# Performance work log

Hardware: AMD Instinct MI355X
Metric: run time of the kernel (lower is better)

The kernel has to match this reference:

```python
import jax, jax.numpy as jnp
import numpy as np

DENSE_SHAPE = (256, 3, 3, 256)  # (out_channels, kh, kw, in_channels)
STRIDES = (1, 1)


def _unfold_nchw(x, kh, kw, sh, sw):
    """torch.nn.functional.unfold layout: rows ordered (C, kh, kw)."""
    B, C, H, W = x.shape
    oh = (H - kh) // sh + 1
    ow = (W - kw) // sw + 1
    # [B, C, kh*kw, oh, ow]; small python loop over 3x3 kernel taps only
    patches = jnp.stack(
        [x[:, :, i:i + sh * oh:sh, j:j + sw * ow:sw]
         for i in range(kh) for j in range(kw)], axis=2)
    return patches.reshape(B, C * kh * kw, oh * ow), oh, ow


def setup_inputs() -> dict:
    key = jax.random.key(0)
    k1, k2, k3, k4, k5, k6 = jax.random.split(key, 6)
    O, kh, kw, C = DENSE_SHAPE
    nnz = 2048
    inp = jax.random.normal(k1, (4, 128, 128, C), dtype=jnp.float32)
    # per-column index ranges for COO weight indices [nnz, 4]
    io = jax.random.randint(k2, (nnz, 1), 0, O)
    ih = jax.random.randint(k3, (nnz, 1), 0, kh)
    iw = jax.random.randint(k4, (nnz, 1), 0, kw)
    ic = jax.random.randint(k5, (nnz, 1), 0, C)
    weight_indices = jnp.concatenate([io, ih, iw, ic], axis=1).astype(jnp.int64)
    weight_values = jax.random.normal(k6, (nnz,), dtype=jnp.float32)
    return {"input": inp, "weight_indices": weight_indices,
            "weight_values": weight_values}


def reference(input, weight_indices, weight_values):
    O, kh, kw, C = DENSE_SHAPE
    sh, sw = STRIDES
    B = input.shape[0]
    # densify COO weight (duplicates are summed, matching coalesce)
    W = jnp.zeros(DENSE_SHAPE, dtype=weight_values.dtype).at[
        weight_indices[:, 0], weight_indices[:, 1],
        weight_indices[:, 2], weight_indices[:, 3]].add(weight_values)
    x = jnp.transpose(input, (0, 3, 1, 2))  # NHWC -> NCHW
    U, oh, ow = _unfold_nchw(x, kh, kw, sh, sw)  # [B, C*kh*kw, oh*ow]
    # NOTE: faithful to the original: weight flattened in (kh,kw,C) order
    # while unfold rows are in (C,kh,kw) order -- same raw matmul.
    out = jnp.einsum('ok,bkl->bol', W.reshape(O, -1), U)
    out = out.reshape(B, O, oh, ow)
    return jnp.transpose(out, (0, 2, 3, 1))  # -> NHWC
```

## Files before the change

kernel.cpp:

```cpp
#include <hip/hip_runtime.h>
#include <cstdint>

#define H_IN   128
#define W_IN   128
#define C_IN   256
#define O_OUT  256
#define OH     126
#define OW     126

#define TY     16
#define TX     4
#define IR     (TY + 2)
#define ICOLS  (TX + 2)
#define NPIX   (IR * ICOLS)
#define SHW    258
#define IN_HW  (NPIX * SHW)
#define NWAVES 8
#define OPW    32
#define SST    34
#define STG_W  (64 * SST)
#define LDS_BYTES (NWAVES * STG_W * 4)

__global__ void prep_kernel(const int* __restrict__ wi, const float* __restrict__ wv,
                            int nnz, int* __restrict__ sgS, int* __restrict__ sgBase,
                            int2* __restrict__ tab) {
    __shared__ int cnt[256];
    __shared__ int smax[32];
    __shared__ int sbase[33];
    __shared__ int is32;
    const int tid = threadIdx.x;
    cnt[tid] = 0;
    if (tid == 0) is32 = 0;
    __syncthreads();
    int f = 0;
    for (int idx = tid * 2 + 1; idx < nnz * 4; idx += 512) f |= wi[idx];
    if (f) atomicOr(&is32, 1);
    __syncthreads();
    const int stride = is32 ? 4 : 8;
    const int step   = is32 ? 1 : 2;
    for (int e = tid; e < nnz; e += 256)
        atomicAdd(&cnt[wi[e * stride]], 1);
    __syncthreads();
    if (tid < 32) {
        int m = 0;
        for (int k = 0; k < 8; ++k) m = max(m, cnt[tid * 8 + k]);
        smax[tid] = m;
    }
    __syncthreads();
    if (tid == 0) {
        int s = 0;
        for (int i = 0; i < 32; ++i) { sbase[i] = s; s += 8 * smax[i]; }
        sbase[32] = s;
    }
    __syncthreads();
    const int T = sbase[32];
    for (int i = tid; i < T; i += 256) tab[i] = make_int2(0, 0);
    cnt[tid] = 0;
    __syncthreads();
    for (int e = tid; e < nnz; e += 256) {
        int o  = wi[e * stride];
        int h  = wi[e * stride + 1 * step];
        int w_ = wi[e * stride + 2 * step];
        int c  = wi[e * stride + 3 * step];
        int k   = h * 768 + w_ * 256 + c;
        int cp  = k / 9;
        int rem = k - cp * 9;
        int i_  = rem / 3;
        int j_  = rem - i_ * 3;
        int meta2 = (((i_ * ICOLS + j_) * SHW) + cp) * 2;
        int slot = atomicAdd(&cnt[o], 1);
        tab[sbase[o >> 3] + slot * 8 + (o & 7)] = make_int2(meta2, __float_as_int(wv[e]));
    }
    if (tid < 32) sgS[tid] = smax[tid];
    if (tid < 33) sgBase[tid] = sbase[tid];
}

__device__ inline unsigned short rtne_bf16(float f) {
    unsigned u = __float_as_uint(f);
    u += 0x7FFFu + ((u >> 16) & 1u);
    return (unsigned short)(u >> 16);
}

__device__ __forceinline__ float bfld(const char* b, int off) {
    return __uint_as_float(((unsigned)*(const unsigned short*)(b + off)) << 16);
}

__global__ __launch_bounds__(512, 4)
void conv_kernel(const float* __restrict__ in, float* __restrict__ out,
                 const int* __restrict__ sgS, const int* __restrict__ sgBase,
                 const int2* __restrict__ tab) {
    extern __shared__ char smem[];
    unsigned short* ldsH = (unsigned short*)smem;
    float*          ldsF = (float*)smem;

    const int tid  = threadIdx.x;
    const int w    = tid >> 6;
    const int lane = tid & 63;
    const int tx = blockIdx.x, ty = blockIdx.y, b = blockIdx.z;
    const int iy0 = ty * TY, ix0 = tx * TX;
    const float* inb = in + (size_t)b * (H_IN * W_IN * C_IN);

    for (int p = w; p < NPIX; p += NWAVES) {
        int r = p / ICOLS, c = p - r * ICOLS;
        int gy = iy0 + r, gx = ix0 + c;
        if (gy < H_IN && gx < W_IN) {
            const float4 v = *(const float4*)(inb + ((gy * W_IN + gx) << 8) + (lane << 2));
            ushort2 lo, hi;
            lo.x = rtne_bf16(v.x); lo.y = rtne_bf16(v.y);
            hi.x = rtne_bf16(v.z); hi.y = rtne_bf16(v.w);
            unsigned short* d = ldsH + p * SHW + (lane << 2);
            *(ushort2*)(d)     = lo;
            *(ushort2*)(d + 2) = hi;
        }
    }
    __syncthreads();

    const int A2  = (((lane >> 2) * ICOLS + (lane & 3)) * SHW) * 2;
    const int sgb = w * 4;
    const char* basep = (const char*)smem;
    float acc[OPW];
#pragma unroll
    for (int i = 0; i < OPW; ++i) acc[i] = 0.f;

#pragma unroll
    for (int g = 0; g < 4; ++g) {
        const int S = sgS[sgb + g];
        const int2* Tg = tab + sgBase[sgb + g];
        for (int slot = 0; slot < S; ++slot) {
            const int4* R = (const int4*)(Tg + (slot << 3));
            const int4 p0 = R[0];
            const int4 p1 = R[1];
            const int4 p2 = R[2];
            const int4 p3 = R[3];
            acc[g * 8 + 0] += __int_as_float(p0.y) * bfld(basep, A2 + p0.x);
            acc[g * 8 + 1] += __int_as_float(p0.w) * bfld(basep, A2 + p0.z);
            acc[g * 8 + 2] += __int_as_float(p1.y) * bfld(basep, A2 + p1.x);
            acc[g * 8 + 3] += __int_as_float(p1.w) * bfld(basep, A2 + p1.z);
            acc[g * 8 + 4] += __int_as_float(p2.y) * bfld(basep, A2 + p2.x);
            acc[g * 8 + 5] += __int_as_float(p2.w) * bfld(basep, A2 + p2.z);
            acc[g * 8 + 6] += __int_as_float(p3.y) * bfld(basep, A2 + p3.x);
            acc[g * 8 + 7] += __int_as_float(p3.w) * bfld(basep, A2 + p3.z);
        }
    }

    __syncthreads();
    const int ob = w * OPW;
    {
        float* st = ldsF + w * STG_W + lane * SST;
#pragma unroll
        for (int k = 0; k < OPW; k += 2)
            *(float2*)(st + k) = make_float2(acc[k], acc[k + 1]);
    }
    __syncthreads();
    {
        const int a_  = lane >> 3;
        const int chq = lane & 7;
        const float* rb = ldsF + w * STG_W;
#pragma unroll
        for (int s8 = 0; s8 < 8; ++s8) {
            int p = s8 * 8 + a_;
            float2 u0 = *(const float2*)(rb + p * SST + chq * 4);
            float2 u1 = *(const float2*)(rb + p * SST + chq * 4 + 2);
            int poy = iy0 + (p >> 2), pox = ix0 + (p & 3);
            if (poy < OH && pox < OW) {
                float4 o4 = make_float4(u0.x, u0.y, u1.x, u1.y);
                *(float4*)(out + (((size_t)b * OH + poy) * OW + pox) * O_OUT + ob + chq * 4) = o4;
            }
        }
    }
}

extern "C" void kernel_launch(void* const* d_in, const int* in_sizes, int n_in,
                              void* d_out, int out_size, void* d_ws, size_t ws_size,
                              hipStream_t stream) {
    const float* input = (const float*)d_in[0];
    const int*   widx  = (const int*)d_in[1];
    const float* wval  = (const float*)d_in[2];
    float* outp = (float*)d_out;
    const int nnz = in_sizes[2];
    const int B = in_sizes[0] / (H_IN * W_IN * C_IN);

    int*  sgS    = (int*)d_ws;
    int*  sgBase = sgS + 32;
    int2* tab    = (int2*)((char*)d_ws + 512);

    prep_kernel<<<1, 256, 0, stream>>>(widx, wval, nnz, sgS, sgBase, tab);

    static_assert(LDS_BYTES >= NPIX * SHW * 2, "flush stage must cover input region");
    static_assert(LDS_BYTES <= 80 * 1024, "need 2 blocks/CU");
    hipFuncSetAttribute((const void*)conv_kernel,
                        hipFuncAttributeMaxDynamicSharedMemorySize, LDS_BYTES);
    dim3 grid((OW + TX - 1) / TX, (OH + TY - 1) / TY, B);
    conv_kernel<<<grid, 512, LDS_BYTES, stream>>>(input, outp, sgS, sgBase, tab);
}
```

Measured before the change: 174.7 us.

## Use 8x8 tiles, shrink LDS to input region, two-pass flush for three blocks/CU

```diff
diff --git a/kernel.cpp b/kernel.cpp
--- a/kernel.cpp
+++ b/kernel.cpp
@@ -8,18 +8,19 @@
 #define OH     126
 #define OW     126
 
-#define TY     16
-#define TX     4
+#define TY     8
+#define TX     8
 #define IR     (TY + 2)
 #define ICOLS  (TX + 2)
 #define NPIX   (IR * ICOLS)
 #define SHW    258
-#define IN_HW  (NPIX * SHW)
+#define IN_BYTES (NPIX * SHW * 2)
 #define NWAVES 8
 #define OPW    32
 #define SST    34
 #define STG_W  (64 * SST)
-#define LDS_BYTES (NWAVES * STG_W * 4)
+#define FLUSH_BYTES (4 * STG_W * 4)
+#define LDS_BYTES IN_BYTES
 
 __global__ void prep_kernel(const int* __restrict__ wi, const float* __restrict__ wv,
                             int nnz, int* __restrict__ sgS, int* __restrict__ sgBase,
@@ -85,7 +86,7 @@
     return __uint_as_float(((unsigned)*(const unsigned short*)(b + off)) << 16);
 }
 
-__global__ __launch_bounds__(512, 4)
+__global__ __launch_bounds__(512, 6)
 void conv_kernel(const float* __restrict__ in, float* __restrict__ out,
                  const int* __restrict__ sgS, const int* __restrict__ sgBase,
                  const int2* __restrict__ tab) {
@@ -94,28 +95,44 @@
     float*          ldsF = (float*)smem;
 
     const int tid  = threadIdx.x;
-    const int w    = tid >> 6;
+    const int w    = __builtin_amdgcn_readfirstlane(tid >> 6);
     const int lane = tid & 63;
     const int tx = blockIdx.x, ty = blockIdx.y, b = blockIdx.z;
     const int iy0 = ty * TY, ix0 = tx * TX;
     const float* inb = in + (size_t)b * (H_IN * W_IN * C_IN);
 
-    for (int p = w; p < NPIX; p += NWAVES) {
-        int r = p / ICOLS, c = p - r * ICOLS;
-        int gy = iy0 + r, gx = ix0 + c;
-        if (gy < H_IN && gx < W_IN) {
-            const float4 v = *(const float4*)(inb + ((gy * W_IN + gx) << 8) + (lane << 2));
-            ushort2 lo, hi;
-            lo.x = rtne_bf16(v.x); lo.y = rtne_bf16(v.y);
-            hi.x = rtne_bf16(v.z); hi.y = rtne_bf16(v.w);
-            unsigned short* d = ldsH + p * SHW + (lane << 2);
-            *(ushort2*)(d)     = lo;
-            *(ushort2*)(d + 2) = hi;
-        }
-    }
-    __syncthreads();
-
-    const int A2  = (((lane >> 2) * ICOLS + (lane & 3)) * SHW) * 2;
+    for (int base = 0; base < 16; base += 4) {
+        float4 v[4];
+#pragma unroll
+        for (int q = 0; q < 4; ++q) {
+            int p = w + (base + q) * NWAVES;
+            if (p < NPIX) {
+                int r = p / ICOLS, c = p - r * ICOLS;
+                int gy = iy0 + r, gx = ix0 + c;
+                if (gy < H_IN && gx < W_IN)
+                    v[q] = *(const float4*)(inb + ((gy * W_IN + gx) << 8) + (lane << 2));
+            }
+        }
+#pragma unroll
+        for (int q = 0; q < 4; ++q) {
+            int p = w + (base + q) * NWAVES;
+            if (p < NPIX) {
+                int r = p / ICOLS, c = p - r * ICOLS;
+                int gy = iy0 + r, gx = ix0 + c;
+                if (gy < H_IN && gx < W_IN) {
+                    ushort2 lo, hi;
+                    lo.x = rtne_bf16(v[q].x); lo.y = rtne_bf16(v[q].y);
+                    hi.x = rtne_bf16(v[q].z); hi.y = rtne_bf16(v[q].w);
+                    unsigned short* d = ldsH + p * SHW + (lane << 2);
+                    *(ushort2*)(d)     = lo;
+                    *(ushort2*)(d + 2) = hi;
+                }
+            }
+        }
+    }
+    __syncthreads();
+
+    const int A2  = (((lane >> 3) * ICOLS + (lane & 7)) * SHW) * 2;
     const int sgb = w * 4;
     const char* basep = (const char*)smem;
     float acc[OPW];
@@ -145,23 +162,48 @@
 
     __syncthreads();
     const int ob = w * OPW;
-    {
-        float* st = ldsF + w * STG_W + lane * SST;
+    const int wq = w & 3;
+    if (w < 4) {
+        float* st = ldsF + wq * STG_W + lane * SST;
 #pragma unroll
         for (int k = 0; k < OPW; k += 2)
             *(float2*)(st + k) = make_float2(acc[k], acc[k + 1]);
     }
     __syncthreads();
-    {
+    if (w < 4) {
         const int a_  = lane >> 3;
         const int chq = lane & 7;
-        const float* rb = ldsF + w * STG_W;
+        const float* rb = ldsF + wq * STG_W;
 #pragma unroll
         for (int s8 = 0; s8 < 8; ++s8) {
             int p = s8 * 8 + a_;
             float2 u0 = *(const float2*)(rb + p * SST + chq * 4);
             float2 u1 = *(const float2*)(rb + p * SST + chq * 4 + 2);
-            int poy = iy0 + (p >> 2), pox = ix0 + (p & 3);
+            int poy = iy0 + (p >> 3), pox = ix0 + (p & 7);
+            if (poy < OH && pox < OW) {
+                float4 o4 = make_float4(u0.x, u0.y, u1.x, u1.y);
+                *(float4*)(out + (((size_t)b * OH + poy) * OW + pox) * O_OUT + ob + chq * 4) = o4;
+            }
+        }
+    }
+    __syncthreads();
+    if (w >= 4) {
+        float* st = ldsF + wq * STG_W + lane * SST;
+#pragma unroll
+        for (int k = 0; k < OPW; k += 2)
+            *(float2*)(st + k) = make_float2(acc[k], acc[k + 1]);
+    }
+    __syncthreads();
+    if (w >= 4) {
+        const int a_  = lane >> 3;
+        const int chq = lane & 7;
+        const float* rb = ldsF + wq * STG_W;
+#pragma unroll
+        for (int s8 = 0; s8 < 8; ++s8) {
+            int p = s8 * 8 + a_;
+            float2 u0 = *(const float2*)(rb + p * SST + chq * 4);
+            float2 u1 = *(const float2*)(rb + p * SST + chq * 4 + 2);
+            int poy = iy0 + (p >> 3), pox = ix0 + (p & 7);
             if (poy < OH && pox < OW) {
                 float4 o4 = make_float4(u0.x, u0.y, u1.x, u1.y);
                 *(float4*)(out + (((size_t)b * OH + poy) * OW + pox) * O_OUT + ob + chq * 4) = o4;
@@ -186,8 +228,8 @@
 
     prep_kernel<<<1, 256, 0, stream>>>(widx, wval, nnz, sgS, sgBase, tab);
 
-    static_assert(LDS_BYTES >= NPIX * SHW * 2, "flush stage must cover input region");
-    static_assert(LDS_BYTES <= 80 * 1024, "need 2 blocks/CU");
+    static_assert(LDS_BYTES >= FLUSH_BYTES, "flush pass must fit in input region");
+    static_assert(3 * LDS_BYTES <= 160 * 1024, "need 3 blocks/CU");
     hipFuncSetAttribute((const void*)conv_kernel,
                         hipFuncAttributeMaxDynamicSharedMemorySize, LDS_BYTES);
     dim3 grid((OW + TX - 1) / TX, (OH + TY - 1) / TY, B);
```

Result: faster. 149.6 us (-14.3%).
